# Kernel tuning notes

Measured on AMD Instinct MI355X. Metric: run time of the kernel, lower is better.

The kernel has to match this reference:

```python
import jax, jax.numpy as jnp
import numpy as np

D_MODEL = 1024
H = 16
D_K = D_MODEL // H
D_FF = 4096
EPS = 1e-6


def layer_norm(x, alpha, bias):
    mean = jnp.mean(x, axis=-1, keepdims=True)
    var = jnp.mean((x - mean) ** 2, axis=-1, keepdims=True)  # unbiased=False
    return alpha * (x - mean) / jnp.sqrt(var + EPS) + bias


def setup_inputs() -> dict:
    key = jax.random.key(0)
    ks = jax.random.split(key, 8)
    B, S = 4, 2048
    sd = 1.0 / np.sqrt(D_MODEL)
    x = jax.random.normal(ks[0], (B, S, D_MODEL), dtype=jnp.float32)
    src_mask = jnp.ones((B, 1, S), dtype=jnp.int32)
    wq = jax.random.normal(ks[1], (D_MODEL, D_MODEL), jnp.float32) * sd
    wk = jax.random.normal(ks[2], (D_MODEL, D_MODEL), jnp.float32) * sd
    wv = jax.random.normal(ks[3], (D_MODEL, D_MODEL), jnp.float32) * sd
    wo = jax.random.normal(ks[4], (D_MODEL, D_MODEL), jnp.float32) * sd
    w1 = jax.random.normal(ks[5], (D_FF, D_MODEL), jnp.float32) * sd
    b1 = jnp.zeros((D_FF,), jnp.float32)
    w2 = jax.random.normal(ks[6], (D_MODEL, D_FF), jnp.float32) * (1.0 / np.sqrt(D_FF))
    b2 = jnp.zeros((D_MODEL,), jnp.float32)
    ln1_a = jnp.ones((D_MODEL,), jnp.float32)
    ln1_b = jnp.zeros((D_MODEL,), jnp.float32)
    ln2_a = jnp.ones((D_MODEL,), jnp.float32)
    ln2_b = jnp.zeros((D_MODEL,), jnp.float32)
    return dict(x=x, src_mask=src_mask, wq=wq, wk=wk, wv=wv, wo=wo,
                ln1_a=ln1_a, ln1_b=ln1_b, ln2_a=ln2_a, ln2_b=ln2_b,
                w1=w1, b1=b1, w2=w2, b2=b2)


def attention(xn, wq, wk, wv, wo, src_mask):
    B, S, _ = xn.shape
    # torch nn.Linear: y = x @ W.T
    q = (xn @ wq.T).reshape(B, S, H, D_K).transpose(0, 2, 1, 3)  # [B,H,S,Dk]
    k = (xn @ wk.T).reshape(B, S, H, D_K).transpose(0, 2, 1, 3)
    v = (xn @ wv.T).reshape(B, S, H, D_K).transpose(0, 2, 1, 3)
    scores = jnp.einsum('bhqd,bhkd->bhqk', q, k) / np.sqrt(D_K)
    m = src_mask[:, None, :, :]  # [B,1,1,S] from [B,1,S]
    scores = jnp.where(m == 0, -jnp.inf, scores)
    attn = jax.nn.softmax(scores, axis=-1)
    out = jnp.einsum('bhqk,bhkd->bhqd', attn, v)
    out = out.transpose(0, 2, 1, 3).reshape(B, S, D_MODEL)
    return out @ wo.T


def reference(x, src_mask, wq, wk, wv, wo, ln1_a, ln1_b, ln2_a, ln2_b, w1, b1, w2, b2):
    # pre-LN residual 1: self-attention
    xn = layer_norm(x, ln1_a, ln1_b)
    x = x + attention(xn, wq, wk, wv, wo, src_mask)
    # pre-LN residual 2: FFN
    xn = layer_norm(x, ln2_a, ln2_b)
    h = jax.nn.relu(xn @ w1.T + b1)
    x = x + (h @ w2.T + b2)
    return x
```

## Files before the change

### kernel.cpp

```cpp
#include <hip/hip_runtime.h>
#include <stdint.h>

typedef unsigned short u16;
typedef __bf16 bf16x8 __attribute__((ext_vector_type(8)));
typedef float   f32x4 __attribute__((ext_vector_type(4)));
typedef u16     u16x8 __attribute__((ext_vector_type(8)));
typedef u16     u16x4 __attribute__((ext_vector_type(4)));

__device__ __forceinline__ float bf2f(u16 u) {
    union { uint32_t i; float f; } c; c.i = ((uint32_t)u) << 16; return c.f;
}
__device__ __forceinline__ u16 f2bf(float f) {
    union { float f; uint32_t i; } c; c.f = f;
    uint32_t r = c.i + 0x7FFFu + ((c.i >> 16) & 1u);
    return (u16)(r >> 16);
}
__device__ __forceinline__ u16 f2bf_fast(float f) {
    union { float f; uint32_t i; } c; c.f = f;
    return (u16)((c.i + 0x8000u) >> 16);
}
__device__ __forceinline__ uint32_t cvt_pk_bf16(float lo, float hi) {
    uint32_t r;
    asm("v_cvt_pk_bf16_f32 %0, %1, %2" : "=v"(r) : "v"(lo), "v"(hi));
    return r;
}
__device__ __forceinline__ void gload_lds16(const u16* g, u16* l) {
    __builtin_amdgcn_global_load_lds(
        (__attribute__((address_space(1))) void*)(g),
        (__attribute__((address_space(3))) void*)(l), 16, 0, 0);
}

__global__ __launch_bounds__(256) void cvt_all(
    const float* __restrict__ wq, const float* __restrict__ wk,
    const float* __restrict__ wv, const float* __restrict__ wo,
    const float* __restrict__ w1, const float* __restrict__ w2,
    u16* __restrict__ wqb, u16* __restrict__ wkb, u16* __restrict__ wvb,
    u16* __restrict__ wob, u16* __restrict__ w1b, u16* __restrict__ w2b)
{
    int blk = blockIdx.x;
    const float* src; u16* dst; int off;
    if      (blk < 1024)  { src = wq; dst = wqb; off = blk; }
    else if (blk < 2048)  { src = wk; dst = wkb; off = blk - 1024; }
    else if (blk < 3072)  { src = wv; dst = wvb; off = blk - 2048; }
    else if (blk < 4096)  { src = wo; dst = wob; off = blk - 3072; }
    else if (blk < 8192)  { src = w1; dst = w1b; off = blk - 4096; }
    else                  { src = w2; dst = w2b; off = blk - 8192; }
    int i = off * 1024 + threadIdx.x * 4;
    float4 v = *(const float4*)(src + i);
    u16x4 o; o[0] = f2bf(v.x); o[1] = f2bf(v.y); o[2] = f2bf(v.z); o[3] = f2bf(v.w);
    *(u16x4*)(dst + i) = o;
}

__global__ __launch_bounds__(256) void ln_kernel(
    const float* __restrict__ x, const float* __restrict__ ga,
    const float* __restrict__ be, u16* __restrict__ out)
{
    const int D = 1024;
    int row  = blockIdx.x * 4 + (threadIdx.x >> 6);
    int lane = threadIdx.x & 63;
    const float* xr = x + (size_t)row * D + lane * 16;
    float f[16];
#pragma unroll
    for (int i = 0; i < 4; ++i) *(float4*)&f[i * 4] = *(const float4*)(xr + i * 4);
    float s = 0.f, s2 = 0.f;
#pragma unroll
    for (int i = 0; i < 16; ++i) { s += f[i]; s2 += f[i] * f[i]; }
#pragma unroll
    for (int off = 1; off < 64; off <<= 1) {
        s  += __shfl_xor(s,  off, 64);
        s2 += __shfl_xor(s2, off, 64);
    }
    float mean = s * (1.0f / 1024.0f);
    float var  = s2 * (1.0f / 1024.0f) - mean * mean;
    var = var < 0.f ? 0.f : var;
    float inv = 1.0f / sqrtf(var + 1e-6f);
    float g[16], b[16];
#pragma unroll
    for (int i = 0; i < 4; ++i) {
        *(float4*)&g[i * 4] = *(const float4*)(ga + lane * 16 + i * 4);
        *(float4*)&b[i * 4] = *(const float4*)(be + lane * 16 + i * 4);
    }
    u16x8 o0, o1;
#pragma unroll
    for (int i = 0; i < 8; ++i) {
        o0[i] = f2bf(g[i]     * (f[i]     - mean) * inv + b[i]);
        o1[i] = f2bf(g[8 + i] * (f[8 + i] - mean) * inv + b[8 + i]);
    }
    u16* orow = out + (size_t)row * D + lane * 16;
    *(u16x8*)(orow)     = o0;
    *(u16x8*)(orow + 8) = o1;
}

__device__ __forceinline__ void gemm_core(
    const u16* __restrict__ A, const u16* __restrict__ W,
    int K, int ldw, int row_a0, int row_w0,
    u16* As, u16* Bs, f32x4 (&acc)[4][4])
{
    int tid  = threadIdx.x;
    int lane = tid & 63;
    int quad = (lane >> 4), l16 = lane & 15;
    int wave = tid >> 6;
    int wr = wave >> 1, wc = wave & 1;
    int srow = tid >> 2, scol = (tid & 3) * 8;
    const u16* a0p = A + (size_t)(row_a0 + srow) * K + scol;
    const u16* a1p = a0p + (size_t)64 * K;
    const u16* b0p = W + (size_t)(row_w0 + srow) * ldw + scol;
    const u16* b1p = b0p + (size_t)64 * ldw;
    u16* la0 = As + tid * 8;
    u16* la1 = As + 2048 + tid * 8;
    u16* la2 = As + 4096 + tid * 8;
    u16* la3 = As + 6144 + tid * 8;
    u16* lb0 = Bs + tid * 8;
    u16* lb1 = Bs + 2048 + tid * 8;
    u16* lb2 = Bs + 4096 + tid * 8;
    u16* lb3 = Bs + 6144 + tid * 8;

    for (int k0 = 0; k0 < K; k0 += 64) {
        __syncthreads();
        gload_lds16(a0p + k0,      la0);
        gload_lds16(a1p + k0,      la1);
        gload_lds16(a0p + k0 + 32, la2);
        gload_lds16(a1p + k0 + 32, la3);
        gload_lds16(b0p + k0,      lb0);
        gload_lds16(b1p + k0,      lb1);
        gload_lds16(b0p + k0 + 32, lb2);
        gload_lds16(b1p + k0 + 32, lb3);
        __syncthreads();
#pragma unroll
        for (int h = 0; h < 2; ++h) {
            const u16* Ah = As + h * 4096;
            const u16* Bh = Bs + h * 4096;
            bf16x8 af[4], bf[4];
#pragma unroll
            for (int mt = 0; mt < 4; ++mt)
                af[mt] = *(const bf16x8*)(&Ah[(wr * 64 + mt * 16 + l16) * 32 + quad * 8]);
#pragma unroll
            for (int nt = 0; nt < 4; ++nt)
                bf[nt] = *(const bf16x8*)(&Bh[(wc * 64 + nt * 16 + l16) * 32 + quad * 8]);
#pragma unroll
            for (int mt = 0; mt < 4; ++mt)
#pragma unroll
                for (int nt = 0; nt < 4; ++nt)
                    acc[mt][nt] = __builtin_amdgcn_mfma_f32_16x16x32_bf16(
                        af[mt], bf[nt], acc[mt][nt], 0, 0, 0);
        }
    }
}

template<bool OUTF32>
__global__ __launch_bounds__(256) void gemm128(
    const u16* __restrict__ A, const u16* __restrict__ W,
    const float* __restrict__ bias, const float* __restrict__ resid,
    void* __restrict__ Cp, int M, int N, int K, int ldw, int do_relu)
{
    __shared__ u16 As[128 * 64];
    __shared__ u16 Bs[128 * 64];
    int tid  = threadIdx.x;
    int lane = tid & 63, wave = tid >> 6;
    int quad = lane >> 4, l16 = lane & 15;
    int wr = wave >> 1, wc = wave & 1;
    const int row_a0 = blockIdx.x * 128, row_w0 = blockIdx.y * 128;
    f32x4 acc[4][4] = {};
    gemm_core(A, W, K, ldw, row_a0, row_w0, As, Bs, acc);
#pragma unroll
    for (int mt = 0; mt < 4; ++mt) {
#pragma unroll
        for (int nt = 0; nt < 4; ++nt) {
#pragma unroll
            for (int r = 0; r < 4; ++r) {
                int grow = row_a0 + wr * 64 + mt * 16 + quad * 4 + r;
                int gcol = row_w0 + wc * 64 + nt * 16 + l16;
                float vv = acc[mt][nt][r];
                if (bias)    vv += bias[gcol];
                if (do_relu) vv = vv > 0.f ? vv : 0.f;
                if (resid)   vv += resid[(size_t)grow * N + gcol];
                if (OUTF32) ((float*)Cp)[(size_t)grow * N + gcol] = vv;
                else        ((u16*)Cp)[(size_t)grow * N + gcol] = f2bf(vv);
            }
        }
    }
}

__global__ __launch_bounds__(256) void gemm128_qkv(
    const u16* __restrict__ A, const u16* __restrict__ Wqkv,
    u16* __restrict__ qo, u16* __restrict__ ko, u16* __restrict__ vo, int K)
{
    __shared__ u16 As[128 * 64];
    __shared__ u16 Bs[128 * 64];
    int tid  = threadIdx.x;
    int lane = tid & 63, wave = tid >> 6;
    int quad = lane >> 4, l16 = lane & 15;
    int wr = wave >> 1, wc = wave & 1;
    const int row_a0 = blockIdx.x * 128, row_w0 = blockIdx.y * 128;
    f32x4 acc[4][4] = {};
    gemm_core(A, Wqkv, K, K, row_a0, row_w0, As, Bs, acc);
    int seg = row_w0 >> 10;
    u16* dst = (seg == 0) ? qo : (seg == 1) ? ko : vo;
    int col0 = row_w0 & 1023;
#pragma unroll
    for (int mt = 0; mt < 4; ++mt) {
#pragma unroll
        for (int nt = 0; nt < 4; ++nt) {
#pragma unroll
            for (int r = 0; r < 4; ++r) {
                int grow = row_a0 + wr * 64 + mt * 16 + quad * 4 + r;
                int gcol = col0 + wc * 64 + nt * 16 + l16;
                dst[(size_t)grow * 1024 + gcol] = f2bf(acc[mt][nt][r]);
            }
        }
    }
}

__global__ __launch_bounds__(512, 4) void attn_kernel(
    const u16* __restrict__ Q, const u16* __restrict__ Km, const u16* __restrict__ Vm,
    const int* __restrict__ mask, u16* __restrict__ O)
{
    const int S = 2048, DM = 1024;
    const float C1 = 0.18033688f;
    const float C0 = -11.541560f;
    __shared__ u16 smem[27136];
    u16* Qs  = smem;
    u16* Ks1 = smem;
    u16* Vt1 = smem + 4096;
    u16* Ks0 = smem + 9216;
    u16* Vt0 = smem + 13312;
    u16* Ps  = smem + 17920;

    int qt = blockIdx.x, bh = blockIdx.y;
    int b = bh >> 4, h = bh & 15;
    int tid = threadIdx.x;
    int wave = tid >> 6, lane = tid & 63;
    int quad = lane >> 4, l16 = lane & 15;
    size_t base = (size_t)b * S;
    size_t hoff = (size_t)h * 64;

    {
        int r = tid >> 2, c0 = (tid & 3) * 16;
        const u16* src = Q + (base + qt * 128 + r) * DM + hoff + c0;
        *(u16x8*)(&Qs[r * 72 + c0])     = *(const u16x8*)(src);
        *(u16x8*)(&Qs[r * 72 + c0 + 8]) = *(const u16x8*)(src + 8);
    }
    const u16* ksrc = Km + (base + (tid >> 3)) * DM + hoff
                    + ((tid & 7) ^ ((tid >> 5) & 7)) * 8;
    int kp = tid & 31, d0 = (tid >> 5) * 4;
    const u16* vsrc = Vm + (base + kp * 2) * DM + hoff + d0;
    const int* msrc = mask + b * S + 4 * l16;

    __syncthreads();
    const int q0 = wave * 16;
    bf16x8 qf0 = *(const bf16x8*)(&Qs[(q0 + l16) * 72 + quad * 8]);
    bf16x8 qf1 = *(const bf16x8*)(&Qs[(q0 + l16) * 72 + 32 + quad * 8]);
    const int swz = (l16 & 7) * 8;
    const int u0  = (quad * 8) ^ swz;

    {
        u16x4 va = *(const u16x4*)(vsrc);
        u16x4 vb = *(const u16x4*)(vsrc + DM);
        gload_lds16(ksrc, Ks0 + tid * 8);
        ksrc += 64 * DM; vsrc += 64 * DM;
#pragma unroll
        for (int i = 0; i < 4; ++i) {
            uint32_t w = (uint32_t)va[i] | ((uint32_t)vb[i] << 16);
            *(uint32_t*)(&Vt0[(d0 + i) * 72 + kp * 2]) = w;
        }
    }
    __syncthreads();

    float l_r[4] = {0.f, 0.f, 0.f, 0.f};
    f32x4 o[4] = {};

    for (int it = 0; it < 32; ++it) {
        const u16* Kcur = (it & 1) ? Ks1 : Ks0;
        const u16* Vcur = (it & 1) ? Vt1 : Vt0;
        u16* Knxt = (it & 1) ? Ks0 : Ks1;
        u16* Vnxt = (it & 1) ? Vt0 : Vt1;
        const bool pfch = (it < 31);
        u16x4 va, vb;
        if (pfch) {
            va = *(const u16x4*)(vsrc);
            vb = *(const u16x4*)(vsrc + DM);
            gload_lds16(ksrc, Knxt + tid * 8);
            ksrc += 64 * DM; vsrc += 64 * DM;
        }
        f32x4 sc[4] = {};
#pragma unroll
        for (int t = 0; t < 4; ++t) {
            const u16* krp = Kcur + (4 * l16 + t) * 64;
            bf16x8 kf0 = *(const bf16x8*)(krp + u0);
            bf16x8 kf1 = *(const bf16x8*)(krp + (u0 ^ 32));
            sc[t] = __builtin_amdgcn_mfma_f32_16x16x32_bf16(qf0, kf0, sc[t], 0, 0, 0);
            sc[t] = __builtin_amdgcn_mfma_f32_16x16x32_bf16(qf1, kf1, sc[t], 0, 0, 0);
        }
        int4 mk4 = *(const int4*)(msrc); msrc += 64;
        float c0t[4];
        c0t[0] = (mk4.x == 0) ? -1e38f : C0;
        c0t[1] = (mk4.y == 0) ? -1e38f : C0;
        c0t[2] = (mk4.z == 0) ? -1e38f : C0;
        c0t[3] = (mk4.w == 0) ? -1e38f : C0;
#pragma unroll
        for (int r = 0; r < 4; ++r) {
            float p0 = exp2f(fmaf(sc[0][r], C1, c0t[0]));
            float p1 = exp2f(fmaf(sc[1][r], C1, c0t[1]));
            float p2 = exp2f(fmaf(sc[2][r], C1, c0t[2]));
            float p3 = exp2f(fmaf(sc[3][r], C1, c0t[3]));
            l_r[r] += (p0 + p1) + (p2 + p3);
            int prow = q0 + quad * 4 + r;
            uint2 pw;
            pw.x = cvt_pk_bf16(p0, p1);
            pw.y = cvt_pk_bf16(p2, p3);
            *(uint2*)(&Ps[prow * 72 + 4 * l16]) = pw;
        }
        bf16x8 pf0 = *(const bf16x8*)(&Ps[(q0 + l16) * 72 + quad * 8]);
        bf16x8 pf1 = *(const bf16x8*)(&Ps[(q0 + l16) * 72 + 32 + quad * 8]);
#pragma unroll
        for (int t = 0; t < 4; ++t) {
            bf16x8 vf0 = *(const bf16x8*)(&Vcur[(t * 16 + l16) * 72 + quad * 8]);
            bf16x8 vf1 = *(const bf16x8*)(&Vcur[(t * 16 + l16) * 72 + 32 + quad * 8]);
            o[t] = __builtin_amdgcn_mfma_f32_16x16x32_bf16(pf0, vf0, o[t], 0, 0, 0);
            o[t] = __builtin_amdgcn_mfma_f32_16x16x32_bf16(pf1, vf1, o[t], 0, 0, 0);
        }
        if (pfch) {
#pragma unroll
            for (int i = 0; i < 4; ++i) {
                uint32_t w = (uint32_t)va[i] | ((uint32_t)vb[i] << 16);
                *(uint32_t*)(&Vnxt[(d0 + i) * 72 + kp * 2]) = w;
            }
        }
        __syncthreads();
    }
#pragma unroll
    for (int r = 0; r < 4; ++r) {
#pragma unroll
        for (int off = 1; off < 16; off <<= 1) l_r[r] += __shfl_xor(l_r[r], off, 16);
        float inv = 1.0f / l_r[r];
        u16* dst = O + (base + qt * 128 + q0 + quad * 4 + r) * DM + hoff + l16;
#pragma unroll
        for (int t = 0; t < 4; ++t) dst[t * 16] = f2bf(o[t][r] * inv);
    }
}

extern "C" void kernel_launch(void* const* d_in, const int* in_sizes, int n_in,
                              void* d_out, int out_size, void* d_ws, size_t ws_size,
                              hipStream_t stream)
{
    (void)in_sizes; (void)n_in; (void)out_size; (void)ws_size;
    const float* x    = (const float*)d_in[0];
    const int*   mask = (const int*)d_in[1];
    const float* wq   = (const float*)d_in[2];
    const float* wk   = (const float*)d_in[3];
    const float* wv   = (const float*)d_in[4];
    const float* wo   = (const float*)d_in[5];
    const float* ln1a = (const float*)d_in[6];
    const float* ln1b = (const float*)d_in[7];
    const float* ln2a = (const float*)d_in[8];
    const float* ln2b = (const float*)d_in[9];
    const float* w1   = (const float*)d_in[10];
    const float* b1   = (const float*)d_in[11];
    const float* w2   = (const float*)d_in[12];
    const float* b2   = (const float*)d_in[13];

    const int M = 8192, D = 1024, F = 4096;
    char* ws = (char*)d_ws;
    u16*  wqkv = (u16*)(ws);
    u16*  wqb = wqkv;
    u16*  wkb = (u16*)(ws + (2u  << 20));
    u16*  wvb = (u16*)(ws + (4u  << 20));
    u16*  wob = (u16*)(ws + (6u  << 20));
    u16*  w1b = (u16*)(ws + (8u  << 20));
    u16*  w2b = (u16*)(ws + (16u << 20));
    u16*  xn  = (u16*)(ws + (24u << 20));
    u16*  q   = (u16*)(ws + (40u << 20));
    u16*  hb  = (u16*)(ws + (40u << 20));

    u16*   kbuf = (u16*)d_out;
    u16*   vbuf = (u16*)d_out + (size_t)M * D;
    float* x1   = (float*)d_out;

    cvt_all<<<12288, 256, 0, stream>>>(wq, wk, wv, wo, w1, w2,
                                       wqb, wkb, wvb, wob, w1b, w2b);

    ln_kernel<<<M / 4, 256, 0, stream>>>(x, ln1a, ln1b, xn);
    dim3 gq(M / 128, 3072 / 128);
    gemm128_qkv<<<gq, 256, 0, stream>>>(xn, wqkv, q, kbuf, vbuf, D);
    dim3 ga(2048 / 128, 64);
    attn_kernel<<<ga, 512, 0, stream>>>(q, kbuf, vbuf, mask, xn);
    dim3 g1(M / 128, D / 128);
    gemm128<true ><<<g1, 256, 0, stream>>>(xn, wob, nullptr, x, x1, M, D, D, D, 0);
    ln_kernel<<<M / 4, 256, 0, stream>>>(x1, ln2a, ln2b, xn);
    dim3 gf1(M / 128, 2048 / 128);
    dim3 gf2(M / 128, D / 128);
    gemm128<false><<<gf1, 256, 0, stream>>>(xn, w1b, b1, nullptr, hb, M, 2048, D, D, 1);
    gemm128<true ><<<gf2, 256, 0, stream>>>(hb, w2b, nullptr, x1, x1, M, D, 2048, F, 0);
    gemm128<false><<<gf1, 256, 0, stream>>>(xn, w1b + (size_t)2048 * D, b1 + 2048, nullptr, hb, M, 2048, D, D, 1);
    gemm128<true ><<<gf2, 256, 0, stream>>>(hb, w2b + 2048, b2, x1, x1, M, D, 2048, F, 0);
}
```

Before: 637.8 us.

## Double attention query tile to 256 rows per block for K/V reuse

Each wave of the attention kernel now processes 32 query rows instead of 16, so a block covers 256 queries and the grid along the query axis is halved. Every K/V tile loaded into LDS is reused by twice as many MFMAs, which halves global K/V traffic and the number of barriers per unit of work. In exchange it needs more registers (two score and output accumulator sets) and more LDS, and it launches half as many blocks, 512, which may reduce occupancy and latency hiding.

```diff
diff --git a/kernel.cpp b/kernel.cpp
--- a/kernel.cpp
+++ b/kernel.cpp
@@ -218,13 +218,13 @@
     const int S = 2048, DM = 1024;
     const float C1 = 0.18033688f;
     const float C0 = -11.541560f;
-    __shared__ u16 smem[27136];
-    u16* Qs  = smem;
-    u16* Ks1 = smem;
-    u16* Vt1 = smem + 4096;
-    u16* Ks0 = smem + 9216;
-    u16* Vt0 = smem + 13312;
-    u16* Ps  = smem + 17920;
+    __shared__ u16 smem[35840];
+    u16* Ks0 = smem;
+    u16* Ks1 = smem + 4096;
+    u16* Vt0 = smem + 8192;
+    u16* Vt1 = smem + 12800;
+    u16* Ps  = smem + 17408;
+    u16* Qs  = smem + 17408;
 
     int qt = blockIdx.x, bh = blockIdx.y;
     int b = bh >> 4, h = bh & 15;
@@ -235,10 +235,13 @@
     size_t hoff = (size_t)h * 64;
 
     {
-        int r = tid >> 2, c0 = (tid & 3) * 16;
-        const u16* src = Q + (base + qt * 128 + r) * DM + hoff + c0;
-        *(u16x8*)(&Qs[r * 72 + c0])     = *(const u16x8*)(src);
-        *(u16x8*)(&Qs[r * 72 + c0 + 8]) = *(const u16x8*)(src + 8);
+        int r = tid >> 1, c0 = (tid & 1) * 32;
+        const u16* src = Q + (base + qt * 256 + r) * DM + hoff + c0;
+        u16* dq = Qs + r * 72 + c0;
+        *(u16x8*)(dq)      = *(const u16x8*)(src);
+        *(u16x8*)(dq + 8)  = *(const u16x8*)(src + 8);
+        *(u16x8*)(dq + 16) = *(const u16x8*)(src + 16);
+        *(u16x8*)(dq + 24) = *(const u16x8*)(src + 24);
     }
     const u16* ksrc = Km + (base + (tid >> 3)) * DM + hoff
                     + ((tid & 7) ^ ((tid >> 5) & 7)) * 8;
@@ -247,9 +250,11 @@
     const int* msrc = mask + b * S + 4 * l16;
 
     __syncthreads();
-    const int q0 = wave * 16;
-    bf16x8 qf0 = *(const bf16x8*)(&Qs[(q0 + l16) * 72 + quad * 8]);
-    bf16x8 qf1 = *(const bf16x8*)(&Qs[(q0 + l16) * 72 + 32 + quad * 8]);
+    const int q0 = wave * 32;
+    bf16x8 qf00 = *(const bf16x8*)(&Qs[(q0 + l16) * 72 + quad * 8]);
+    bf16x8 qf01 = *(const bf16x8*)(&Qs[(q0 + l16) * 72 + 32 + quad * 8]);
+    bf16x8 qf10 = *(const bf16x8*)(&Qs[(q0 + 16 + l16) * 72 + quad * 8]);
+    bf16x8 qf11 = *(const bf16x8*)(&Qs[(q0 + 16 + l16) * 72 + 32 + quad * 8]);
     const int swz = (l16 & 7) * 8;
     const int u0  = (quad * 8) ^ swz;
 
@@ -266,8 +271,9 @@
     }
     __syncthreads();
 
-    float l_r[4] = {0.f, 0.f, 0.f, 0.f};
-    f32x4 o[4] = {};
+    float l0[4] = {0.f, 0.f, 0.f, 0.f};
+    float l1[4] = {0.f, 0.f, 0.f, 0.f};
+    f32x4 o0[4] = {}, o1[4] = {};
 
     for (int it = 0; it < 32; ++it) {
         const u16* Kcur = (it & 1) ? Ks1 : Ks0;
@@ -282,14 +288,16 @@
             gload_lds16(ksrc, Knxt + tid * 8);
             ksrc += 64 * DM; vsrc += 64 * DM;
         }
-        f32x4 sc[4] = {};
+        f32x4 s0[4] = {}, s1[4] = {};
 #pragma unroll
         for (int t = 0; t < 4; ++t) {
             const u16* krp = Kcur + (4 * l16 + t) * 64;
             bf16x8 kf0 = *(const bf16x8*)(krp + u0);
             bf16x8 kf1 = *(const bf16x8*)(krp + (u0 ^ 32));
-            sc[t] = __builtin_amdgcn_mfma_f32_16x16x32_bf16(qf0, kf0, sc[t], 0, 0, 0);
-            sc[t] = __builtin_amdgcn_mfma_f32_16x16x32_bf16(qf1, kf1, sc[t], 0, 0, 0);
+            s0[t] = __builtin_amdgcn_mfma_f32_16x16x32_bf16(qf00, kf0, s0[t], 0, 0, 0);
+            s0[t] = __builtin_amdgcn_mfma_f32_16x16x32_bf16(qf01, kf1, s0[t], 0, 0, 0);
+            s1[t] = __builtin_amdgcn_mfma_f32_16x16x32_bf16(qf10, kf0, s1[t], 0, 0, 0);
+            s1[t] = __builtin_amdgcn_mfma_f32_16x16x32_bf16(qf11, kf1, s1[t], 0, 0, 0);
         }
         int4 mk4 = *(const int4*)(msrc); msrc += 64;
         float c0t[4];
@@ -299,25 +307,40 @@
         c0t[3] = (mk4.w == 0) ? -1e38f : C0;
 #pragma unroll
         for (int r = 0; r < 4; ++r) {
-            float p0 = exp2f(fmaf(sc[0][r], C1, c0t[0]));
-            float p1 = exp2f(fmaf(sc[1][r], C1, c0t[1]));
-            float p2 = exp2f(fmaf(sc[2][r], C1, c0t[2]));
-            float p3 = exp2f(fmaf(sc[3][r], C1, c0t[3]));
-            l_r[r] += (p0 + p1) + (p2 + p3);
-            int prow = q0 + quad * 4 + r;
+            float p0 = exp2f(fmaf(s0[0][r], C1, c0t[0]));
+            float p1 = exp2f(fmaf(s0[1][r], C1, c0t[1]));
+            float p2 = exp2f(fmaf(s0[2][r], C1, c0t[2]));
+            float p3 = exp2f(fmaf(s0[3][r], C1, c0t[3]));
+            l0[r] += (p0 + p1) + (p2 + p3);
             uint2 pw;
             pw.x = cvt_pk_bf16(p0, p1);
             pw.y = cvt_pk_bf16(p2, p3);
-            *(uint2*)(&Ps[prow * 72 + 4 * l16]) = pw;
-        }
-        bf16x8 pf0 = *(const bf16x8*)(&Ps[(q0 + l16) * 72 + quad * 8]);
-        bf16x8 pf1 = *(const bf16x8*)(&Ps[(q0 + l16) * 72 + 32 + quad * 8]);
+            *(uint2*)(&Ps[(q0 + quad * 4 + r) * 72 + 4 * l16]) = pw;
+        }
+#pragma unroll
+        for (int r = 0; r < 4; ++r) {
+            float p0 = exp2f(fmaf(s1[0][r], C1, c0t[0]));
+            float p1 = exp2f(fmaf(s1[1][r], C1, c0t[1]));
+            float p2 = exp2f(fmaf(s1[2][r], C1, c0t[2]));
+            float p3 = exp2f(fmaf(s1[3][r], C1, c0t[3]));
+            l1[r] += (p0 + p1) + (p2 + p3);
+            uint2 pw;
+            pw.x = cvt_pk_bf16(p0, p1);
+            pw.y = cvt_pk_bf16(p2, p3);
+            *(uint2*)(&Ps[(q0 + 16 + quad * 4 + r) * 72 + 4 * l16]) = pw;
+        }
+        bf16x8 pf00 = *(const bf16x8*)(&Ps[(q0 + l16) * 72 + quad * 8]);
+        bf16x8 pf01 = *(const bf16x8*)(&Ps[(q0 + l16) * 72 + 32 + quad * 8]);
+        bf16x8 pf10 = *(const bf16x8*)(&Ps[(q0 + 16 + l16) * 72 + quad * 8]);
+        bf16x8 pf11 = *(const bf16x8*)(&Ps[(q0 + 16 + l16) * 72 + 32 + quad * 8]);
 #pragma unroll
         for (int t = 0; t < 4; ++t) {
             bf16x8 vf0 = *(const bf16x8*)(&Vcur[(t * 16 + l16) * 72 + quad * 8]);
             bf16x8 vf1 = *(const bf16x8*)(&Vcur[(t * 16 + l16) * 72 + 32 + quad * 8]);
-            o[t] = __builtin_amdgcn_mfma_f32_16x16x32_bf16(pf0, vf0, o[t], 0, 0, 0);
-            o[t] = __builtin_amdgcn_mfma_f32_16x16x32_bf16(pf1, vf1, o[t], 0, 0, 0);
+            o0[t] = __builtin_amdgcn_mfma_f32_16x16x32_bf16(pf00, vf0, o0[t], 0, 0, 0);
+            o0[t] = __builtin_amdgcn_mfma_f32_16x16x32_bf16(pf01, vf1, o0[t], 0, 0, 0);
+            o1[t] = __builtin_amdgcn_mfma_f32_16x16x32_bf16(pf10, vf0, o1[t], 0, 0, 0);
+            o1[t] = __builtin_amdgcn_mfma_f32_16x16x32_bf16(pf11, vf1, o1[t], 0, 0, 0);
         }
         if (pfch) {
 #pragma unroll
@@ -331,11 +354,19 @@
 #pragma unroll
     for (int r = 0; r < 4; ++r) {
 #pragma unroll
-        for (int off = 1; off < 16; off <<= 1) l_r[r] += __shfl_xor(l_r[r], off, 16);
-        float inv = 1.0f / l_r[r];
-        u16* dst = O + (base + qt * 128 + q0 + quad * 4 + r) * DM + hoff + l16;
-#pragma unroll
-        for (int t = 0; t < 4; ++t) dst[t * 16] = f2bf(o[t][r] * inv);
+        for (int off = 1; off < 16; off <<= 1) {
+            l0[r] += __shfl_xor(l0[r], off, 16);
+            l1[r] += __shfl_xor(l1[r], off, 16);
+        }
+        float i0 = 1.0f / l0[r];
+        float i1 = 1.0f / l1[r];
+        u16* dst0 = O + (base + qt * 256 + q0 + quad * 4 + r) * DM + hoff + l16;
+        u16* dst1 = dst0 + (size_t)16 * DM;
+#pragma unroll
+        for (int t = 0; t < 4; ++t) {
+            dst0[t * 16] = f2bf(o0[t][r] * i0);
+            dst1[t * 16] = f2bf(o1[t][r] * i1);
+        }
     }
 }
 
@@ -382,7 +413,7 @@
     ln_kernel<<<M / 4, 256, 0, stream>>>(x, ln1a, ln1b, xn);
     dim3 gq(M / 128, 3072 / 128);
     gemm128_qkv<<<gq, 256, 0, stream>>>(xn, wqkv, q, kbuf, vbuf, D);
-    dim3 ga(2048 / 128, 64);
+    dim3 ga(2048 / 256, 64);
     attn_kernel<<<ga, 512, 0, stream>>>(q, kbuf, vbuf, mask, xn);
     dim3 g1(M / 128, D / 128);
     gemm128<true ><<<g1, 256, 0, stream>>>(xn, wob, nullptr, x, x1, M, D, D, D, 0);
```

Measured after the change: 620.7 us. 2.7% less time.
